# Kernel tuning notes

Hardware: AMD Instinct MI355X
Metric: run time of the kernel (lower is better)

## Reference

```python
import jax, jax.numpy as jnp
import numpy as np

B, S, D, H, F, V, K = 8, 1024, 1024, 16, 4096, 8192, 64
HD = D // H
ALPHA = 0.1


def layernorm(x, g, b, eps=1e-5):
    mu = jnp.mean(x, axis=-1, keepdims=True)
    var = jnp.var(x, axis=-1, keepdims=True)
    return (x - mu) * jax.lax.rsqrt(var + eps) * g + b


def setup_inputs() -> dict:
    key = jax.random.key(0)
    ks = jax.random.split(key, 16)
    s = lambda fan: 1.0 / np.sqrt(fan)
    inp = {
        "x": jax.random.normal(ks[0], (B, S, D), jnp.float32),
        "token_ids": jax.random.randint(ks[1], (B, S), 0, V),
        "pmi": jax.random.normal(ks[2], (V, V), jnp.float32) * 0.1,
        "Wq": jax.random.normal(ks[3], (D, D), jnp.float32) * s(D),
        "bq": jnp.zeros((D,), jnp.float32),
        "Wk": jax.random.normal(ks[4], (D, D), jnp.float32) * s(D),
        "bk": jnp.zeros((D,), jnp.float32),
        "Wv": jax.random.normal(ks[5], (D, D), jnp.float32) * s(D),
        "bv": jnp.zeros((D,), jnp.float32),
        "Wo": jax.random.normal(ks[6], (D, D), jnp.float32) * s(D),
        "bo": jnp.zeros((D,), jnp.float32),
        "W1": jax.random.normal(ks[7], (D, F), jnp.float32) * s(D),
        "b1": jnp.zeros((F,), jnp.float32),
        "W2": jax.random.normal(ks[8], (F, D), jnp.float32) * s(F),
        "b2": jnp.zeros((D,), jnp.float32),
        "g1": jnp.ones((D,), jnp.float32),
        "be1": jnp.zeros((D,), jnp.float32),
        "g2": jnp.ones((D,), jnp.float32),
        "be2": jnp.zeros((D,), jnp.float32),
    }
    return inp


def reference(x, token_ids, pmi, Wq, bq, Wk, bk, Wv, bv, Wo, bo,
              W1, b1, W2, b2, g1, be1, g2, be2):
    # --- SparseStatAttention: QK^T + alpha*PMI bias, top-k mask, softmax ---
    q = (x @ Wq + bq).reshape(B, S, H, HD)
    k = (x @ Wk + bk).reshape(B, S, H, HD)
    v = (x @ Wv + bv).reshape(B, S, H, HD)
    scores = jnp.einsum("bihd,bjhd->bhij", q, k) / np.sqrt(HD)  # [B,H,S,S]
    bias = pmi[token_ids[:, :, None], token_ids[:, None, :]]     # [B,S,S]
    scores = scores + ALPHA * bias[:, None, :, :]
    # top-k sparsification per query row (threshold at k-th largest value)
    kth = jax.lax.top_k(scores, K)[0][..., -1:]
    scores = jnp.where(scores >= kth, scores, -jnp.inf)
    w = jax.nn.softmax(scores, axis=-1)
    attn = jnp.einsum("bhij,bjhd->bihd", w, v).reshape(B, S, D)
    attn = attn @ Wo + bo
    # --- residual + norm1 (dropout is identity in eval) ---
    h = layernorm(x + attn, g1, be1)
    # --- GELU FFN (torch nn.GELU default = exact erf) ---
    ff = jax.nn.gelu(h @ W1 + b1, approximate=False) @ W2 + b2
    return layernorm(h + ff, g2, be2)
```

## Files before the change

### kernel.cpp

```cpp
#include <hip/hip_runtime.h>
#include <cstdint>
#include <cstddef>

#define B_   8
#define S_   1024
#define D_   1024
#define H_   16
#define HD_  64
#define F_   4096
#define V_   8192
#define KTOP 64

typedef unsigned short ushort_t;
typedef __attribute__((ext_vector_type(8))) short short8;
typedef __attribute__((ext_vector_type(8))) _Float16 half8;
typedef __attribute__((ext_vector_type(4))) float floatx4;
typedef __attribute__((ext_vector_type(4))) unsigned int uintx4;
typedef __attribute__((ext_vector_type(4))) float floatv4;
typedef __attribute__((ext_vector_type(4))) unsigned short ushortx4;
typedef __attribute__((ext_vector_type(8))) unsigned short ushortx8;

__device__ __forceinline__ ushort_t f2bf(float f) {
    unsigned int u = __builtin_bit_cast(unsigned int, f);
    u += 0x7fffu + ((u >> 16) & 1u);
    return (ushort_t)(u >> 16);
}
__device__ __forceinline__ float bf2f(ushort_t u) {
    unsigned int x = ((unsigned int)u) << 16;
    return __builtin_bit_cast(float, x);
}
__device__ __forceinline__ ushort_t f2h(float f) {
    _Float16 h = (_Float16)f;
    return __builtin_bit_cast(ushort_t, h);
}
__device__ __forceinline__ float h2f(ushort_t u) {
    return (float)__builtin_bit_cast(_Float16, u);
}

__device__ __forceinline__ void gload_lds16(const ushort_t* g, ushort_t* lds_base) {
    __builtin_amdgcn_global_load_lds(
        (const __attribute__((address_space(1))) unsigned int*)g,
        (__attribute__((address_space(3))) unsigned int*)lds_base,
        16, 0, 0);
}

__global__ __launch_bounds__(256) void cast_x_kernel(const float* __restrict__ x,
                                                     ushort_t* __restrict__ xb) {
    int gid = blockIdx.x * 256 + threadIdx.x;
    floatv4 v = ((const floatv4*)x)[gid];
    ushortx4 o;
    o[0] = f2bf(v[0]); o[1] = f2bf(v[1]); o[2] = f2bf(v[2]); o[3] = f2bf(v[3]);
    ((ushortx4*)xb)[gid] = o;
}

__global__ void transpose_cast_kernel(const float* __restrict__ W, ushort_t* __restrict__ WT,
                                      int K, int N, float scale) {
    __shared__ float tile[32][33];
    int n0 = blockIdx.x * 32, k0 = blockIdx.y * 32;
    #pragma unroll
    for (int i = threadIdx.y; i < 32; i += 8)
        tile[i][threadIdx.x] = W[(size_t)(k0 + i) * N + n0 + threadIdx.x];
    __syncthreads();
    #pragma unroll
    for (int i = threadIdx.y; i < 32; i += 8)
        WT[(size_t)(n0 + i) * K + k0 + threadIdx.x] = f2bf(tile[threadIdx.x][i] * scale);
}

__global__ __launch_bounds__(256) void pack_bias3_kernel(const float* __restrict__ bq,
                                                         const float* __restrict__ bk,
                                                         const float* __restrict__ bv,
                                                         float* __restrict__ o) {
    int i = blockIdx.x * 256 + threadIdx.x;
    float v = (i < 1024) ? bq[i] * 0.125f : (i < 2048) ? bk[i - 1024] : bv[i - 2048];
    o[i] = v;
}

__global__ __launch_bounds__(256) void bias_gather_kernel(const int* __restrict__ tok,
                                                          const float* __restrict__ pmi,
                                                          ushort_t* __restrict__ biasb) {
    int b = blockIdx.x >> 10;
    int i = blockIdx.x & (S_ - 1);
    int ti = tok[b * S_ + i];
    const float* prow = pmi + (size_t)ti * V_;
    #pragma unroll
    for (int it = 0; it < 4; it++) {
        int j = threadIdx.x + it * 256;
        int tj = tok[b * S_ + j];
        biasb[(size_t)blockIdx.x * S_ + j] = f2h(0.1f * prow[tj]);
    }
}

__global__ __launch_bounds__(256) void transpose_v_kernel(const ushort_t* __restrict__ v,
                                                          ushort_t* __restrict__ vT) {
    __shared__ ushort_t t[64 * 72];
    int bh = blockIdx.x >> 4;
    int s0 = (blockIdx.x & 15) * 64;
    #pragma unroll
    for (int it = 0; it < 2; it++) {
        int idx = threadIdx.x + it * 256;
        int sl = idx >> 3, dg = (idx & 7) * 8;
        *(uintx4*)&t[sl * 72 + dg] = *(const uintx4*)&v[((size_t)bh * S_ + s0 + sl) * HD_ + dg];
    }
    __syncthreads();
    #pragma unroll
    for (int it = 0; it < 2; it++) {
        int idx = threadIdx.x + it * 256;
        int dl = idx >> 3, sg = (idx & 7) * 8;
        ushortx8 o;
        #pragma unroll
        for (int i = 0; i < 8; i++) o[i] = f2h(bf2f(t[(sg + i) * 72 + dl]));
        *(ushortx8*)&vT[((size_t)bh * HD_ + dl) * S_ + s0 + sg] = o;
    }
}

__global__ __launch_bounds__(256) void gemm_bt(const ushort_t* __restrict__ A,
                                               const ushort_t* __restrict__ BT,
                                               const float* __restrict__ bias,
                                               ushort_t* __restrict__ C,
                                               int M, int N, int K, int ep) {
    __shared__ ushort_t As[2][128 * 32];
    __shared__ ushort_t Bs[2][128 * 32];

    const int tid = threadIdx.x;
    const int wid = tid >> 6, lane = tid & 63;
    const int quad = lane >> 4, r = lane & 15;
    const int wr = wid >> 1, wc = wid & 1;
    const int m0 = blockIdx.y * 128, n0 = blockIdx.x * 128;

    floatx4 acc[4][4];
    #pragma unroll
    for (int a = 0; a < 4; a++)
        #pragma unroll
        for (int b = 0; b < 4; b++) acc[a][b] = (floatx4){0.f, 0.f, 0.f, 0.f};

    const int srow = wid * 16 + (lane >> 2);
    const int scol = (lane & 3) * 8;
    const ushort_t* Ag0 = A + (size_t)(m0 + srow) * K + scol;
    const ushort_t* Ag1 = A + (size_t)(m0 + 64 + srow) * K + scol;
    const ushort_t* Bg0 = BT + (size_t)(n0 + srow) * K + scol;
    const ushort_t* Bg1 = BT + (size_t)(n0 + 64 + srow) * K + scol;
    const int d0 = (wid * 16) * 32;
    const int d1 = (64 + wid * 16) * 32;

    gload_lds16(Ag0, &As[0][d0]);
    gload_lds16(Ag1, &As[0][d1]);
    gload_lds16(Bg0, &Bs[0][d0]);
    gload_lds16(Bg1, &Bs[0][d1]);
    __syncthreads();

    int cur = 0;
    for (int k0 = 0; k0 < K; k0 += 32) {
        const int nxt = cur ^ 1;
        if (k0 + 32 < K) {
            gload_lds16(Ag0 + k0 + 32, &As[nxt][d0]);
            gload_lds16(Ag1 + k0 + 32, &As[nxt][d1]);
            gload_lds16(Bg0 + k0 + 32, &Bs[nxt][d0]);
            gload_lds16(Bg1 + k0 + 32, &Bs[nxt][d1]);
        }
        short8 af[4], bf[4];
        #pragma unroll
        for (int t = 0; t < 4; t++)
            af[t] = *(const short8*)&As[cur][(wr * 64 + t * 16 + r) * 32 + quad * 8];
        #pragma unroll
        for (int t = 0; t < 4; t++)
            bf[t] = *(const short8*)&Bs[cur][(wc * 64 + t * 16 + r) * 32 + quad * 8];
        #pragma unroll
        for (int tm = 0; tm < 4; tm++)
            #pragma unroll
            for (int tn = 0; tn < 4; tn++)
                acc[tm][tn] = __builtin_amdgcn_mfma_f32_16x16x32_bf16(af[tm], bf[tn], acc[tm][tn], 0, 0, 0);
        __syncthreads();
        cur = nxt;
    }

    #pragma unroll
    for (int tm = 0; tm < 4; tm++) {
        #pragma unroll
        for (int tn = 0; tn < 4; tn++) {
            const int n = n0 + wc * 64 + tn * 16 + r;
            const float bv = bias[n];
            #pragma unroll
            for (int i2 = 0; i2 < 4; i2++) {
                const int m = m0 + wr * 64 + tm * 16 + quad * 4 + i2;
                float v = acc[tm][tn][i2] + bv;
                if (ep == 1) v = 0.5f * v * (1.0f + erff(v * 0.70710678118654752f));
                size_t idx;
                if (ep == 2) {
                    int tensor = n >> 10, nn = n & 1023;
                    idx = (size_t)tensor * (B_ * S_ * D_)
                        + (((size_t)(m >> 10) * H_ + (nn >> 6)) * S_ + (m & (S_ - 1))) * HD_ + (nn & (HD_ - 1));
                } else {
                    idx = (size_t)m * N + n;
                }
                C[idx] = f2bf(v);
            }
        }
    }
}

__global__ __launch_bounds__(512) void attn_kernel(const ushort_t* __restrict__ q,
                                                   const ushort_t* __restrict__ k,
                                                   const ushort_t* __restrict__ vT,
                                                   const ushort_t* __restrict__ biasb,
                                                   ushort_t* __restrict__ attnb) {
    extern __shared__ char smem[];
    ushort_t* Sm = (ushort_t*)smem;
    _Float16* Smh = (_Float16*)smem;

    const int bid = blockIdx.x;
    const int b = bid >> 10;
    const int h = (bid >> 6) & (H_ - 1);
    const int i0 = (bid & 63) * 16;
    const int tid = threadIdx.x;
    const int wid = tid >> 6, lane = tid & 63;
    const int quad = lane >> 4, r = lane & 15;

    const size_t bh = (size_t)b * H_ + h;
    const ushort_t* qbase = q + bh * S_ * HD_;
    const ushort_t* kbase = k + bh * S_ * HD_;
    const ushort_t* vbase = vT + bh * HD_ * S_;
    const ushort_t* bsrc = biasb + ((size_t)b * S_ + i0) * S_;

    #pragma unroll
    for (int c8 = 0; c8 < 4; c8++) {
        int c = wid * 4 + c8;
        int row = c >> 1, half = c & 1;
        int xr = row & 7;
        gload_lds16(bsrc + (size_t)row * S_ + half * 512 + (lane ^ xr) * 8,
                    Sm + row * 1024 + half * 512);
    }
    short8 aq0 = *(const short8*)&qbase[(size_t)(i0 + r) * HD_ + quad * 8];
    short8 aq1 = *(const short8*)&qbase[(size_t)(i0 + r) * HD_ + 32 + quad * 8];
    __syncthreads();

    const int q1 = quad >> 1;
    const int xr0 = r & 7;
    const int labase = r * 1024 + ((((wid & 3) * 2 + q1) ^ xr0) << 3)
                     + ((wid >> 2) << 6) + (quad & 1) * 4;
    const ushort_t* kpl = kbase + (size_t)(wid * 16 + r) * HD_ + quad * 8;
    #pragma unroll
    for (int t = 0; t < 8; t++) {
        const int la = labase + t * 128;
        ushortx4 bi = *(const ushortx4*)&Sm[la];
        floatx4 acc;
        acc[0] = h2f(bi[0]); acc[1] = h2f(bi[1]); acc[2] = h2f(bi[2]); acc[3] = h2f(bi[3]);
        const ushort_t* kp = kpl + (size_t)t * 128 * HD_;
        short8 b0 = *(const short8*)kp;
        short8 b1 = *(const short8*)(kp + 32);
        acc = __builtin_amdgcn_mfma_f32_16x16x32_bf16(b0, aq0, acc, 0, 0, 0);
        acc = __builtin_amdgcn_mfma_f32_16x16x32_bf16(b1, aq1, acc, 0, 0, 0);
        ushortx4 so;
        so[0] = f2h(acc[0]); so[1] = f2h(acc[1]); so[2] = f2h(acc[2]); so[3] = f2h(acc[3]);
        *(ushortx4*)&Sm[la] = so;
    }
    __syncthreads();

    for (int rr = 0; rr < 2; rr++) {
        int row = wid * 2 + rr;
        ushort_t* Srow = Sm + row * 1024;
        ushortx8 u0 = *(const ushortx8*)&Srow[lane * 8];
        ushortx8 u1 = *(const ushortx8*)&Srow[(64 + lane) * 8];
        unsigned int kk[16];
        unsigned int lmax = 0u;
        #pragma unroll
        for (int t = 0; t < 8; t++) {
            unsigned int ua = u0[t];
            kk[t] = ua ^ ((ua & 0x8000u) ? 0xFFFFu : 0x8000u);
            lmax = kk[t] > lmax ? kk[t] : lmax;
            unsigned int ub = u1[t];
            kk[8 + t] = ub ^ ((ub & 0x8000u) ? 0xFFFFu : 0x8000u);
            lmax = kk[8 + t] > lmax ? kk[8 + t] : lmax;
        }
        unsigned int M = lmax, T0 = lmax;
        #pragma unroll
        for (int off = 32; off; off >>= 1) {
            unsigned int om = (unsigned int)__shfl_xor((int)M, off);
            unsigned int ot = (unsigned int)__shfl_xor((int)T0, off);
            M = om > M ? om : M;
            T0 = ot < T0 ? ot : T0;
        }
        float mx = h2f((ushort_t)((M & 0x8000u) ? (M ^ 0x8000u) : (~M & 0xFFFFu)));
        unsigned int T;
        int hb;
        unsigned int diff = T0 ^ M;
        if (diff == 0u) { T = M; hb = -1; }
        else { hb = 31 - __builtin_clz(diff); T = M & ~((2u << hb) - 1u); }
        for (int bit = hb; bit >= 0; bit--) {
            unsigned int trial = T | (1u << bit);
            int c = 0;
            #pragma unroll
            for (int t = 0; t < 16; t++)
                c += __popcll(__ballot(kk[t] >= trial));
            if (c >= KTOP) {
                T = trial;
                if (c == KTOP) break;
            }
        }
        float ev[16]; float sum = 0.f;
        #pragma unroll
        for (int t = 0; t < 8; t++) {
            float sa = h2f((ushort_t)u0[t]);
            float ea = (kk[t] >= T) ? __expf(sa - mx) : 0.f;
            ev[t] = ea; sum += ea;
            float sb = h2f((ushort_t)u1[t]);
            float eb = (kk[8 + t] >= T) ? __expf(sb - mx) : 0.f;
            ev[8 + t] = eb; sum += eb;
        }
        #pragma unroll
        for (int off = 32; off; off >>= 1) sum += __shfl_xor(sum, off);
        float inv = 1.f / sum;
        ushortx8 w0, w1;
        #pragma unroll
        for (int t = 0; t < 8; t++) {
            w0[t] = f2h(ev[t] * inv);
            w1[t] = f2h(ev[8 + t] * inv);
        }
        *(ushortx8*)&Srow[lane * 8] = w0;
        *(ushortx8*)&Srow[(64 + lane) * 8] = w1;
    }
    __syncthreads();

    const int dt = wid & 3, ksh = wid >> 2;
    floatx4 o0 = (floatx4){0.f, 0.f, 0.f, 0.f};
    floatx4 o1 = (floatx4){0.f, 0.f, 0.f, 0.f};
    const _Float16* Srowp = Smh + (size_t)r * 1024;
    const int xr = r & 7;
    const ushort_t* vrow = vbase + (size_t)(dt * 16 + r) * S_;
    #pragma unroll
    for (int kss = 0; kss < 8; kss++) {
        int ks = ksh * 16 + kss * 2;
        half8 wa0 = *(const half8*)&Srowp[((ks * 4 + quad) ^ xr) << 3];
        half8 wa1 = *(const half8*)&Srowp[(((ks + 1) * 4 + quad) ^ xr) << 3];
        half8 vb0 = *(const half8*)&vrow[ks * 32 + quad * 8];
        half8 vb1 = *(const half8*)&vrow[(ks + 1) * 32 + quad * 8];
        o0 = __builtin_amdgcn_mfma_f32_16x16x32_f16(wa0, vb0, o0, 0, 0, 0);
        o1 = __builtin_amdgcn_mfma_f32_16x16x32_f16(wa1, vb1, o1, 0, 0, 0);
    }
    floatx4 oacc = o0 + o1;
    __syncthreads();
    float* red = (float*)smem;
    if (ksh == 1) {
        #pragma unroll
        for (int i2 = 0; i2 < 4; i2++)
            red[dt * 256 + (quad * 4 + i2) * 16 + r] = oacc[i2];
    }
    __syncthreads();
    if (ksh == 0) {
        #pragma unroll
        for (int i2 = 0; i2 < 4; i2++) {
            int row = quad * 4 + i2;
            float v = oacc[i2] + red[dt * 256 + row * 16 + r];
            attnb[((size_t)b * S_ + i0 + row) * D_ + h * HD_ + dt * 16 + r] = f2bf(v);
        }
    }
}

__global__ __launch_bounds__(256) void ln1_kernel(const float* __restrict__ x,
                                                  const ushort_t* __restrict__ t,
                                                  const float* __restrict__ g,
                                                  const float* __restrict__ be,
                                                  ushort_t* __restrict__ hb) {
    int row = blockIdx.x, tid = threadIdx.x;
    const float* xr = x + (size_t)row * D_;
    const ushort_t* tr = t + (size_t)row * D_;
    float v[4]; float s = 0.f, s2 = 0.f;
    #pragma unroll
    for (int it = 0; it < 4; it++) {
        int j = tid + it * 256;
        v[it] = xr[j] + bf2f(tr[j]);
        s += v[it]; s2 += v[it] * v[it];
    }
    #pragma unroll
    for (int off = 32; off; off >>= 1) { s += __shfl_xor(s, off); s2 += __shfl_xor(s2, off); }
    __shared__ float rs[4], rq[4];
    if ((tid & 63) == 0) { rs[tid >> 6] = s; rq[tid >> 6] = s2; }
    __syncthreads();
    s = rs[0] + rs[1] + rs[2] + rs[3];
    s2 = rq[0] + rq[1] + rq[2] + rq[3];
    float mu = s * (1.f / D_);
    float var = s2 * (1.f / D_) - mu * mu;
    float rstd = rsqrtf(var + 1e-5f);
    #pragma unroll
    for (int it = 0; it < 4; it++) {
        int j = tid + it * 256;
        hb[(size_t)row * D_ + j] = f2bf((v[it] - mu) * rstd * g[j] + be[j]);
    }
}

__global__ __launch_bounds__(256) void ln2_kernel(const ushort_t* __restrict__ hbuf,
                                                  const ushort_t* __restrict__ t,
                                                  const float* __restrict__ g,
                                                  const float* __restrict__ be,
                                                  float* __restrict__ out) {
    int row = blockIdx.x, tid = threadIdx.x;
    const ushort_t* hr = hbuf + (size_t)row * D_;
    const ushort_t* tr = t + (size_t)row * D_;
    float v[4]; float s = 0.f, s2 = 0.f;
    #pragma unroll
    for (int it = 0; it < 4; it++) {
        int j = tid + it * 256;
        v[it] = bf2f(hr[j]) + bf2f(tr[j]);
        s += v[it]; s2 += v[it] * v[it];
    }
    #pragma unroll
    for (int off = 32; off; off >>= 1) { s += __shfl_xor(s, off); s2 += __shfl_xor(s2, off); }
    __shared__ float rs[4], rq[4];
    if ((tid & 63) == 0) { rs[tid >> 6] = s; rq[tid >> 6] = s2; }
    __syncthreads();
    s = rs[0] + rs[1] + rs[2] + rs[3];
    s2 = rq[0] + rq[1] + rq[2] + rq[3];
    float mu = s * (1.f / D_);
    float var = s2 * (1.f / D_) - mu * mu;
    float rstd = rsqrtf(var + 1e-5f);
    #pragma unroll
    for (int it = 0; it < 4; it++) {
        int j = tid + it * 256;
        out[(size_t)row * D_ + j] = (v[it] - mu) * rstd * g[j] + be[j];
    }
}

extern "C" void kernel_launch(void* const* d_in, const int* in_sizes, int n_in,
                              void* d_out, int out_size, void* d_ws, size_t ws_size,
                              hipStream_t stream) {
    (void)in_sizes; (void)n_in; (void)out_size; (void)ws_size;
    const float* x   = (const float*)d_in[0];
    const int*   tok = (const int*)d_in[1];
    const float* pmi = (const float*)d_in[2];
    const float* Wq  = (const float*)d_in[3];
    const float* bq  = (const float*)d_in[4];
    const float* Wk  = (const float*)d_in[5];
    const float* bk  = (const float*)d_in[6];
    const float* Wv  = (const float*)d_in[7];
    const float* bv  = (const float*)d_in[8];
    const float* Wo  = (const float*)d_in[9];
    const float* bo  = (const float*)d_in[10];
    const float* W1  = (const float*)d_in[11];
    const float* b1  = (const float*)d_in[12];
    const float* W2  = (const float*)d_in[13];
    const float* b2  = (const float*)d_in[14];
    const float* g1  = (const float*)d_in[15];
    const float* be1 = (const float*)d_in[16];
    const float* g2  = (const float*)d_in[17];
    const float* be2 = (const float*)d_in[18];
    float* out = (float*)d_out;

    char* ws = (char*)d_ws;
    size_t off = 0;
    auto alloc = [&](size_t bytes) { char* p = ws + off; off += (bytes + 255) & ~(size_t)255; return p; };
    const size_t BSD = (size_t)B_ * S_ * D_;
    ushort_t* xb     = (ushort_t*)alloc(BSD * 2);
    ushort_t* WqkvT  = (ushort_t*)alloc((size_t)3 * D_ * D_ * 2);
    ushort_t* WoT    = (ushort_t*)alloc((size_t)D_ * D_ * 2);
    ushort_t* W1T    = (ushort_t*)alloc((size_t)D_ * F_ * 2);
    ushort_t* W2T    = (ushort_t*)alloc((size_t)F_ * D_ * 2);
    float*    bqkv   = (float*)alloc(3072 * 4);
    ushort_t* qkvb   = (ushort_t*)alloc(3 * BSD * 2);
    ushort_t* vT     = (ushort_t*)alloc(BSD * 2);
    ushort_t* biasb  = (ushort_t*)alloc((size_t)B_ * S_ * S_ * 2);
    ushort_t* extra  = (ushort_t*)alloc(BSD * 2);
    (void)extra;
    ushort_t* qb    = qkvb;
    ushort_t* kb    = qkvb + BSD;
    ushort_t* vb    = qkvb + 2 * BSD;
    ushort_t* attnb = xb;
    ushort_t* tbuf  = qb;
    ushort_t* hb    = kb;
    ushort_t* ffb   = vb;

    const size_t attn_lds = 16 * 1024 * 2;

    cast_x_kernel<<<8192, 256, 0, stream>>>(x, xb);
    transpose_cast_kernel<<<dim3(32, 32), dim3(32, 8), 0, stream>>>(Wq, WqkvT, D_, D_, 0.125f);
    transpose_cast_kernel<<<dim3(32, 32), dim3(32, 8), 0, stream>>>(Wk, WqkvT + (size_t)D_ * D_, D_, D_, 1.0f);
    transpose_cast_kernel<<<dim3(32, 32), dim3(32, 8), 0, stream>>>(Wv, WqkvT + (size_t)2 * D_ * D_, D_, D_, 1.0f);
    transpose_cast_kernel<<<dim3(32, 32), dim3(32, 8), 0, stream>>>(Wo, WoT, D_, D_, 1.0f);
    transpose_cast_kernel<<<dim3(128, 32), dim3(32, 8), 0, stream>>>(W1, W1T, D_, F_, 1.0f);
    transpose_cast_kernel<<<dim3(32, 128), dim3(32, 8), 0, stream>>>(W2, W2T, F_, D_, 1.0f);
    pack_bias3_kernel<<<12, 256, 0, stream>>>(bq, bk, bv, bqkv);
    bias_gather_kernel<<<B_ * S_, 256, 0, stream>>>(tok, pmi, biasb);

    gemm_bt<<<dim3(24, 64), 256, 0, stream>>>(xb, WqkvT, bqkv, qkvb, B_ * S_, 3 * D_, D_, 2);
    transpose_v_kernel<<<B_ * H_ * (S_ / 64), 256, 0, stream>>>(vb, vT);

    attn_kernel<<<B_ * H_ * (S_ / 16), 512, attn_lds, stream>>>(qb, kb, vT, biasb, attnb);

    gemm_bt<<<dim3(8, 64), 256, 0, stream>>>(attnb, WoT, bo, tbuf, B_ * S_, D_, D_, 0);
    ln1_kernel<<<B_ * S_, 256, 0, stream>>>(x, tbuf, g1, be1, hb);
    gemm_bt<<<dim3(32, 64), 256, 0, stream>>>(hb, W1T, b1, ffb, B_ * S_, F_, D_, 1);
    gemm_bt<<<dim3(8, 64), 256, 0, stream>>>(ffb, W2T, b2, tbuf, B_ * S_, D_, F_, 0);
    ln2_kernel<<<B_ * S_, 256, 0, stream>>>(hb, tbuf, g2, be2, out);
}
```

Baseline: 1.081 ms.

## Prefetch K/V fragments, interleave two-row top-k selection, use static LDS in attention

Software-pipelines the K loads in the QK^T loop and the V loads in the PV loop by fetching the next iteration's fragments ahead of the MFMAs. The per-wave top-k and softmax now handle both rows at once: packed 16-bit max/min shuffle reductions and interleaved bitwise threshold searches let the two rows' ballots overlap. The softmax exponentials are recomputed rather than kept in an array, and LDS becomes a static array with a launch-bounds occupancy hint. This adds register pressure, which may cause spills or lower occupancy under the 8-waves hint.

```diff
diff --git a/kernel.cpp b/kernel.cpp
--- a/kernel.cpp
+++ b/kernel.cpp
@@ -198,14 +198,13 @@
     }
 }
 
-__global__ __launch_bounds__(512) void attn_kernel(const ushort_t* __restrict__ q,
-                                                   const ushort_t* __restrict__ k,
-                                                   const ushort_t* __restrict__ vT,
-                                                   const ushort_t* __restrict__ biasb,
-                                                   ushort_t* __restrict__ attnb) {
-    extern __shared__ char smem[];
-    ushort_t* Sm = (ushort_t*)smem;
-    _Float16* Smh = (_Float16*)smem;
+__global__ __launch_bounds__(512, 8) void attn_kernel(const ushort_t* __restrict__ q,
+                                                      const ushort_t* __restrict__ k,
+                                                      const ushort_t* __restrict__ vT,
+                                                      const ushort_t* __restrict__ biasb,
+                                                      ushort_t* __restrict__ attnb) {
+    __shared__ ushort_t Sm[16 * 1024];
+    _Float16* Smh = (_Float16*)Sm;
 
     const int bid = blockIdx.x;
     const int b = bid >> 10;
@@ -238,85 +237,126 @@
     const int labase = r * 1024 + ((((wid & 3) * 2 + q1) ^ xr0) << 3)
                      + ((wid >> 2) << 6) + (quad & 1) * 4;
     const ushort_t* kpl = kbase + (size_t)(wid * 16 + r) * HD_ + quad * 8;
+    short8 kb0 = *(const short8*)kpl;
+    short8 kb1 = *(const short8*)(kpl + 32);
     #pragma unroll
     for (int t = 0; t < 8; t++) {
+        short8 kc0, kc1;
+        if (t < 7) {
+            const ushort_t* kp = kpl + (size_t)(t + 1) * 128 * HD_;
+            kc0 = *(const short8*)kp;
+            kc1 = *(const short8*)(kp + 32);
+        }
         const int la = labase + t * 128;
         ushortx4 bi = *(const ushortx4*)&Sm[la];
         floatx4 acc;
         acc[0] = h2f(bi[0]); acc[1] = h2f(bi[1]); acc[2] = h2f(bi[2]); acc[3] = h2f(bi[3]);
-        const ushort_t* kp = kpl + (size_t)t * 128 * HD_;
-        short8 b0 = *(const short8*)kp;
-        short8 b1 = *(const short8*)(kp + 32);
-        acc = __builtin_amdgcn_mfma_f32_16x16x32_bf16(b0, aq0, acc, 0, 0, 0);
-        acc = __builtin_amdgcn_mfma_f32_16x16x32_bf16(b1, aq1, acc, 0, 0, 0);
+        acc = __builtin_amdgcn_mfma_f32_16x16x32_bf16(kb0, aq0, acc, 0, 0, 0);
+        acc = __builtin_amdgcn_mfma_f32_16x16x32_bf16(kb1, aq1, acc, 0, 0, 0);
         ushortx4 so;
         so[0] = f2h(acc[0]); so[1] = f2h(acc[1]); so[2] = f2h(acc[2]); so[3] = f2h(acc[3]);
         *(ushortx4*)&Sm[la] = so;
-    }
-    __syncthreads();
-
-    for (int rr = 0; rr < 2; rr++) {
-        int row = wid * 2 + rr;
-        ushort_t* Srow = Sm + row * 1024;
-        ushortx8 u0 = *(const ushortx8*)&Srow[lane * 8];
-        ushortx8 u1 = *(const ushortx8*)&Srow[(64 + lane) * 8];
-        unsigned int kk[16];
-        unsigned int lmax = 0u;
+        kb0 = kc0; kb1 = kc1;
+    }
+    __syncthreads();
+
+    {
+        const int rowA = wid * 2, rowB = rowA + 1;
+        ushort_t* SA = Sm + rowA * 1024;
+        ushort_t* SB = Sm + rowB * 1024;
+        ushortx8 uA0 = *(const ushortx8*)&SA[lane * 8];
+        ushortx8 uA1 = *(const ushortx8*)&SA[(64 + lane) * 8];
+        ushortx8 uB0 = *(const ushortx8*)&SB[lane * 8];
+        ushortx8 uB1 = *(const ushortx8*)&SB[(64 + lane) * 8];
+        unsigned int kA[16], kB[16];
+        unsigned int lmA = 0u, lmB = 0u;
         #pragma unroll
         for (int t = 0; t < 8; t++) {
-            unsigned int ua = u0[t];
-            kk[t] = ua ^ ((ua & 0x8000u) ? 0xFFFFu : 0x8000u);
-            lmax = kk[t] > lmax ? kk[t] : lmax;
-            unsigned int ub = u1[t];
-            kk[8 + t] = ub ^ ((ub & 0x8000u) ? 0xFFFFu : 0x8000u);
-            lmax = kk[8 + t] > lmax ? kk[8 + t] : lmax;
-        }
-        unsigned int M = lmax, T0 = lmax;
+            unsigned int ua = uA0[t];
+            kA[t] = ua ^ ((ua & 0x8000u) ? 0xFFFFu : 0x8000u);
+            lmA = kA[t] > lmA ? kA[t] : lmA;
+            unsigned int ub = uA1[t];
+            kA[8 + t] = ub ^ ((ub & 0x8000u) ? 0xFFFFu : 0x8000u);
+            lmA = kA[8 + t] > lmA ? kA[8 + t] : lmA;
+            unsigned int uc = uB0[t];
+            kB[t] = uc ^ ((uc & 0x8000u) ? 0xFFFFu : 0x8000u);
+            lmB = kB[t] > lmB ? kB[t] : lmB;
+            unsigned int ud = uB1[t];
+            kB[8 + t] = ud ^ ((ud & 0x8000u) ? 0xFFFFu : 0x8000u);
+            lmB = kB[8 + t] > lmB ? kB[8 + t] : lmB;
+        }
+        unsigned int pmax = (lmA << 16) | lmB;
+        unsigned int pmin = pmax;
         #pragma unroll
         for (int off = 32; off; off >>= 1) {
-            unsigned int om = (unsigned int)__shfl_xor((int)M, off);
-            unsigned int ot = (unsigned int)__shfl_xor((int)T0, off);
-            M = om > M ? om : M;
-            T0 = ot < T0 ? ot : T0;
-        }
-        float mx = h2f((ushort_t)((M & 0x8000u) ? (M ^ 0x8000u) : (~M & 0xFFFFu)));
-        unsigned int T;
-        int hb;
-        unsigned int diff = T0 ^ M;
-        if (diff == 0u) { T = M; hb = -1; }
-        else { hb = 31 - __builtin_clz(diff); T = M & ~((2u << hb) - 1u); }
-        for (int bit = hb; bit >= 0; bit--) {
-            unsigned int trial = T | (1u << bit);
-            int c = 0;
-            #pragma unroll
-            for (int t = 0; t < 16; t++)
-                c += __popcll(__ballot(kk[t] >= trial));
-            if (c >= KTOP) {
-                T = trial;
-                if (c == KTOP) break;
+            unsigned int om = (unsigned int)__shfl_xor((int)pmax, off);
+            unsigned int on = (unsigned int)__shfl_xor((int)pmin, off);
+            unsigned int mh = (om >> 16) > (pmax >> 16) ? (om >> 16) : (pmax >> 16);
+            unsigned int ml = (om & 0xFFFFu) > (pmax & 0xFFFFu) ? (om & 0xFFFFu) : (pmax & 0xFFFFu);
+            pmax = (mh << 16) | ml;
+            unsigned int nh = (on >> 16) < (pmin >> 16) ? (on >> 16) : (pmin >> 16);
+            unsigned int nl = (on & 0xFFFFu) < (pmin & 0xFFFFu) ? (on & 0xFFFFu) : (pmin & 0xFFFFu);
+            pmin = (nh << 16) | nl;
+        }
+        const unsigned int MA = pmax >> 16, MB = pmax & 0xFFFFu;
+        const unsigned int T0A = pmin >> 16, T0B = pmin & 0xFFFFu;
+        const float mxA = h2f((ushort_t)((MA & 0x8000u) ? (MA ^ 0x8000u) : (~MA & 0xFFFFu)));
+        const float mxB = h2f((ushort_t)((MB & 0x8000u) ? (MB ^ 0x8000u) : (~MB & 0xFFFFu)));
+        unsigned int TA, TB; int hbA, hbB;
+        {
+            unsigned int dA = T0A ^ MA;
+            if (dA == 0u) { TA = MA; hbA = -1; }
+            else { hbA = 31 - __builtin_clz(dA); TA = MA & ~((2u << hbA) - 1u); }
+            unsigned int dB = T0B ^ MB;
+            if (dB == 0u) { TB = MB; hbB = -1; }
+            else { hbB = 31 - __builtin_clz(dB); TB = MB & ~((2u << hbB) - 1u); }
+        }
+        bool dnA = (hbA < 0), dnB = (hbB < 0);
+        for (int bit = (hbA > hbB ? hbA : hbB); bit >= 0; bit--) {
+            if (!dnA && bit <= hbA) {
+                unsigned int tr = TA | (1u << bit);
+                int c = 0;
+                #pragma unroll
+                for (int t = 0; t < 16; t++)
+                    c += __popcll(__ballot(kA[t] >= tr));
+                if (c >= KTOP) { TA = tr; if (c == KTOP) dnA = true; }
             }
-        }
-        float ev[16]; float sum = 0.f;
+            if (!dnB && bit <= hbB) {
+                unsigned int tr = TB | (1u << bit);
+                int c = 0;
+                #pragma unroll
+                for (int t = 0; t < 16; t++)
+                    c += __popcll(__ballot(kB[t] >= tr));
+                if (c >= KTOP) { TB = tr; if (c == KTOP) dnB = true; }
+            }
+            if (dnA && dnB) break;
+        }
+        float sA = 0.f, sB = 0.f;
         #pragma unroll
         for (int t = 0; t < 8; t++) {
-            float sa = h2f((ushort_t)u0[t]);
-            float ea = (kk[t] >= T) ? __expf(sa - mx) : 0.f;
-            ev[t] = ea; sum += ea;
-            float sb = h2f((ushort_t)u1[t]);
-            float eb = (kk[8 + t] >= T) ? __expf(sb - mx) : 0.f;
-            ev[8 + t] = eb; sum += eb;
-        }
-        #pragma unroll
-        for (int off = 32; off; off >>= 1) sum += __shfl_xor(sum, off);
-        float inv = 1.f / sum;
-        ushortx8 w0, w1;
+            sA += (kA[t] >= TA)     ? __expf(h2f((ushort_t)uA0[t]) - mxA) : 0.f;
+            sA += (kA[8 + t] >= TA) ? __expf(h2f((ushort_t)uA1[t]) - mxA) : 0.f;
+            sB += (kB[t] >= TB)     ? __expf(h2f((ushort_t)uB0[t]) - mxB) : 0.f;
+            sB += (kB[8 + t] >= TB) ? __expf(h2f((ushort_t)uB1[t]) - mxB) : 0.f;
+        }
+        #pragma unroll
+        for (int off = 32; off; off >>= 1) {
+            sA += __shfl_xor(sA, off);
+            sB += __shfl_xor(sB, off);
+        }
+        const float iA = 1.f / sA, iB = 1.f / sB;
+        ushortx8 wA0, wA1, wB0, wB1;
         #pragma unroll
         for (int t = 0; t < 8; t++) {
-            w0[t] = f2h(ev[t] * inv);
-            w1[t] = f2h(ev[8 + t] * inv);
-        }
-        *(ushortx8*)&Srow[lane * 8] = w0;
-        *(ushortx8*)&Srow[(64 + lane) * 8] = w1;
+            wA0[t] = f2h(((kA[t] >= TA)     ? __expf(h2f((ushort_t)uA0[t]) - mxA) : 0.f) * iA);
+            wA1[t] = f2h(((kA[8 + t] >= TA) ? __expf(h2f((ushort_t)uA1[t]) - mxA) : 0.f) * iA);
+            wB0[t] = f2h(((kB[t] >= TB)     ? __expf(h2f((ushort_t)uB0[t]) - mxB) : 0.f) * iB);
+            wB1[t] = f2h(((kB[8 + t] >= TB) ? __expf(h2f((ushort_t)uB1[t]) - mxB) : 0.f) * iB);
+        }
+        *(ushortx8*)&SA[lane * 8] = wA0;
+        *(ushortx8*)&SA[(64 + lane) * 8] = wA1;
+        *(ushortx8*)&SB[lane * 8] = wB0;
+        *(ushortx8*)&SB[(64 + lane) * 8] = wB1;
     }
     __syncthreads();
 
@@ -325,20 +365,26 @@
     floatx4 o1 = (floatx4){0.f, 0.f, 0.f, 0.f};
     const _Float16* Srowp = Smh + (size_t)r * 1024;
     const int xr = r & 7;
-    const ushort_t* vrow = vbase + (size_t)(dt * 16 + r) * S_;
+    const ushort_t* vrow = vbase + (size_t)(dt * 16 + r) * S_ + (size_t)ksh * 16 * 32 + quad * 8;
+    half8 vb0 = *(const half8*)&vrow[0];
+    half8 vb1 = *(const half8*)&vrow[32];
     #pragma unroll
     for (int kss = 0; kss < 8; kss++) {
+        half8 vc0, vc1;
+        if (kss < 7) {
+            vc0 = *(const half8*)&vrow[(kss + 1) * 64];
+            vc1 = *(const half8*)&vrow[(kss + 1) * 64 + 32];
+        }
         int ks = ksh * 16 + kss * 2;
         half8 wa0 = *(const half8*)&Srowp[((ks * 4 + quad) ^ xr) << 3];
         half8 wa1 = *(const half8*)&Srowp[(((ks + 1) * 4 + quad) ^ xr) << 3];
-        half8 vb0 = *(const half8*)&vrow[ks * 32 + quad * 8];
-        half8 vb1 = *(const half8*)&vrow[(ks + 1) * 32 + quad * 8];
         o0 = __builtin_amdgcn_mfma_f32_16x16x32_f16(wa0, vb0, o0, 0, 0, 0);
         o1 = __builtin_amdgcn_mfma_f32_16x16x32_f16(wa1, vb1, o1, 0, 0, 0);
+        vb0 = vc0; vb1 = vc1;
     }
     floatx4 oacc = o0 + o1;
     __syncthreads();
-    float* red = (float*)smem;
+    float* red = (float*)Sm;
     if (ksh == 1) {
         #pragma unroll
         for (int i2 = 0; i2 < 4; i2++)
@@ -467,8 +513,6 @@
     ushort_t* hb    = kb;
     ushort_t* ffb   = vb;
 
-    const size_t attn_lds = 16 * 1024 * 2;
-
     cast_x_kernel<<<8192, 256, 0, stream>>>(x, xb);
     transpose_cast_kernel<<<dim3(32, 32), dim3(32, 8), 0, stream>>>(Wq, WqkvT, D_, D_, 0.125f);
     transpose_cast_kernel<<<dim3(32, 32), dim3(32, 8), 0, stream>>>(Wk, WqkvT + (size_t)D_ * D_, D_, D_, 1.0f);
@@ -482,7 +526,7 @@
     gemm_bt<<<dim3(24, 64), 256, 0, stream>>>(xb, WqkvT, bqkv, qkvb, B_ * S_, 3 * D_, D_, 2);
     transpose_v_kernel<<<B_ * H_ * (S_ / 64), 256, 0, stream>>>(vb, vT);
 
-    attn_kernel<<<B_ * H_ * (S_ / 16), 512, attn_lds, stream>>>(qb, kb, vT, biasb, attnb);
+    attn_kernel<<<B_ * H_ * (S_ / 16), 512, 0, stream>>>(qb, kb, vT, biasb, attnb);
 
     gemm_bt<<<dim3(8, 64), 256, 0, stream>>>(attnb, WoT, bo, tbuf, B_ * S_, D_, D_, 0);
     ln1_kernel<<<B_ * S_, 256, 0, stream>>>(x, tbuf, g1, be1, hb);
```

Result: slower. 1.111 ms (+2.8%).
